# Kernel optimization log

Measured on AMD Instinct MI355X. Metric: run time of the kernel, lower is better.

Reference implementation:

```python
import jax, jax.numpy as jnp
import numpy as np

BATCH = 1024
D_MODEL = 1024
HEADS = 16
D_K = D_MODEL // HEADS  # 64


def setup_inputs() -> dict:
    key = jax.random.key(0)
    ks = jax.random.split(key, 8)
    s = 1.0 / np.sqrt(D_MODEL)
    return {
        "x": jax.random.normal(ks[0], (BATCH, D_MODEL), dtype=jnp.float32),
        "weights": jax.random.normal(ks[1], (BATCH, HEADS, D_K, D_K), dtype=jnp.float32),
        "Wq": jax.random.normal(ks[2], (D_MODEL, HEADS * D_K), dtype=jnp.float32) * s,
        "Wk": jax.random.normal(ks[3], (D_MODEL, HEADS * D_K), dtype=jnp.float32) * s,
        "Wv": jax.random.normal(ks[4], (D_MODEL, HEADS * D_K), dtype=jnp.float32) * s,
        "Wg": jax.random.normal(ks[5], (D_MODEL, HEADS), dtype=jnp.float32) * s,
        "Wo": jax.random.normal(ks[6], (D_MODEL, D_MODEL), dtype=jnp.float32) * s,
        "bo": jnp.zeros((D_MODEL,), dtype=jnp.float32),
    }


def reference(x, weights, Wq, Wk, Wv, Wg, Wo, bo):
    b = x.shape[0]
    h, dv, dk = weights.shape[1], weights.shape[2], weights.shape[3]
    # projections -> [b, h, d_k]; sigma is identity in this module
    q = (x @ Wq).reshape(b, h, dk)
    k = (x @ Wk).reshape(b, h, dk)
    v = (x @ Wv).reshape(b, h, dv)
    # gate beta: [b, h, 1]
    beta = jax.nn.sigmoid(x @ Wg)[:, :, None]
    # read existing value from fast-weight memory
    v_existing = jnp.einsum('bhvk,bhk->bhv', weights, k)
    # outer-product delta-rule write
    new_weights = weights + jnp.einsum('bhv,bhk->bhvk', beta * (v - v_existing), k)
    # read with query
    out = jnp.einsum('bhvk,bhk->bhv', new_weights, q).reshape(b, h * dv)
    out = out @ Wo + bo
    return (out, new_weights)
```

## Files before the change

### kernel.cpp

```cpp
#include <hip/hip_runtime.h>

#define BATCH 1024
#define DMODEL 1024
#define HEADS 16

typedef short bh8 __attribute__((ext_vector_type(8)));
typedef float f4 __attribute__((ext_vector_type(4)));
typedef unsigned short u16x4 __attribute__((ext_vector_type(4)));

__device__ inline unsigned short f2b(float f) {
  union { float f; unsigned int u; } x; x.f = f;
  unsigned int r = x.u + 0x7fffu + ((x.u >> 16) & 1u);
  return (unsigned short)(r >> 16);
}

__global__ __launch_bounds__(256)
void cvt_bf16_kernel(const float* __restrict__ in, unsigned short* __restrict__ out, int n4) {
  int i = blockIdx.x * 256 + threadIdx.x;
  if (i >= n4) return;
  const float4 f = ((const float4*)in)[i];
  u16x4 h = { f2b(f.x), f2b(f.y), f2b(f.z), f2b(f.w) };
  ((u16x4*)out)[i] = h;
}

__global__ __launch_bounds__(256)
void transpose_cvt_kernel(const float* __restrict__ in, unsigned short* __restrict__ out,
                          int R, int C) {
  __shared__ float t[32][33];
  int c0 = blockIdx.x * 32, r0 = blockIdx.y * 32;
  int tx = threadIdx.x, ty = threadIdx.y;
  #pragma unroll
  for (int i = ty; i < 32; i += 8)
    t[i][tx] = in[(size_t)(r0 + i) * C + c0 + tx];
  __syncthreads();
  #pragma unroll
  for (int i = ty; i < 32; i += 8)
    out[(size_t)(c0 + i) * R + r0 + tx] = f2b(t[tx][i]);
}

__global__ __launch_bounds__(256)
void beta_kernel(const float* __restrict__ x, const float* __restrict__ Wg,
                 float* __restrict__ beta) {
  __shared__ float xr[DMODEL];
  int b = blockIdx.x;
  for (int i = threadIdx.x; i < DMODEL; i += 256) xr[i] = x[(size_t)b * DMODEL + i];
  __syncthreads();
  int wid = threadIdx.x >> 6, lane = threadIdx.x & 63;
  #pragma unroll
  for (int hh = 0; hh < 4; ++hh) {
    int h = wid * 4 + hh;
    float p = 0.f;
    for (int i = lane; i < DMODEL; i += 64) p += xr[i] * Wg[(size_t)i * HEADS + h];
    #pragma unroll
    for (int off = 32; off > 0; off >>= 1) p += __shfl_down(p, off, 64);
    if (lane == 0) beta[b * HEADS + h] = 1.f / (1.f + __expf(-p));
  }
}

template<int BM, int BN>
__global__ __launch_bounds__(256)
void gemm_tn(const unsigned short* __restrict__ A, const unsigned short* __restrict__ Bt,
             float* __restrict__ C, const float* __restrict__ bias, int N, int K) {
  constexpr int BK = 32;
  constexpr int LD = BK + 8;
  constexpr int TM = BM / 32;
  constexpr int TN = BN / 32;
  __shared__ unsigned short As[BM * LD];
  __shared__ unsigned short Bs[BN * LD];
  const int tid = threadIdx.x;
  const int lane = tid & 63;
  const int wid = tid >> 6;
  const int wm = wid >> 1, wn = wid & 1;
  const int m0 = blockIdx.y * BM, n0 = blockIdx.x * BN;
  const int row16 = lane & 15;
  const int quad = lane >> 4;
  const int s_chunk = tid & 3, s_row = tid >> 2;

  f4 acc[TM][TN];
  #pragma unroll
  for (int i = 0; i < TM; ++i)
    #pragma unroll
    for (int j = 0; j < TN; ++j)
      acc[i][j] = f4{0.f, 0.f, 0.f, 0.f};

  for (int k0 = 0; k0 < K; k0 += BK) {
    #pragma unroll
    for (int p = 0; p < BM / 64; ++p) {
      int r = s_row + p * 64;
      bh8 v = *(const bh8*)(A + (size_t)(m0 + r) * K + k0 + s_chunk * 8);
      *(bh8*)(&As[r * LD + s_chunk * 8]) = v;
    }
    #pragma unroll
    for (int p = 0; p < BN / 64; ++p) {
      int r = s_row + p * 64;
      bh8 v = *(const bh8*)(Bt + (size_t)(n0 + r) * K + k0 + s_chunk * 8);
      *(bh8*)(&Bs[r * LD + s_chunk * 8]) = v;
    }
    __syncthreads();
    bh8 af[TM], bfr[TN];
    #pragma unroll
    for (int i = 0; i < TM; ++i)
      af[i] = *(const bh8*)(&As[(wm * (BM / 2) + i * 16 + row16) * LD + quad * 8]);
    #pragma unroll
    for (int j = 0; j < TN; ++j)
      bfr[j] = *(const bh8*)(&Bs[(wn * (BN / 2) + j * 16 + row16) * LD + quad * 8]);
    #pragma unroll
    for (int i = 0; i < TM; ++i)
      #pragma unroll
      for (int j = 0; j < TN; ++j)
        acc[i][j] = __builtin_amdgcn_mfma_f32_16x16x32_bf16(af[i], bfr[j], acc[i][j], 0, 0, 0);
    __syncthreads();
  }
  #pragma unroll
  for (int i = 0; i < TM; ++i) {
    #pragma unroll
    for (int j = 0; j < TN; ++j) {
      int col = n0 + wn * (BN / 2) + j * 16 + row16;
      float bv = bias ? bias[col] : 0.f;
      #pragma unroll
      for (int rg = 0; rg < 4; ++rg) {
        int row = m0 + wm * (BM / 2) + i * 16 + quad * 4 + rg;
        C[(size_t)row * N + col] = acc[i][j][rg] + bv;
      }
    }
  }
}

__global__ __launch_bounds__(256)
void fastweight_kernel(const float* __restrict__ Wf, const float* __restrict__ QKV,
                       const float* __restrict__ beta, float* __restrict__ newW,
                       unsigned short* __restrict__ hiddenh) {
  const int bh = blockIdx.x;
  const int b = bh >> 4, h = bh & 15;
  const int tid = threadIdx.x;
  const int r = tid >> 2, q4 = tid & 3;
  const float* base = QKV + (size_t)b * 3072 + h * 64;
  const float4* qp = (const float4*)base;
  const float4* kp = (const float4*)(base + 1024);
  const float* vp = base + 2048;
  const float be = beta[bh];
  const size_t woff = (size_t)bh * 4096 + (size_t)r * 64 + q4 * 16;
  const float4* wp = (const float4*)(Wf + woff);
  float4 w[4], kk[4];
  #pragma unroll
  for (int i = 0; i < 4; ++i) w[i] = wp[i];
  #pragma unroll
  for (int i = 0; i < 4; ++i) kk[i] = kp[q4 * 4 + i];
  float vex = 0.f;
  #pragma unroll
  for (int i = 0; i < 4; ++i)
    vex += w[i].x * kk[i].x + w[i].y * kk[i].y + w[i].z * kk[i].z + w[i].w * kk[i].w;
  vex += __shfl_xor(vex, 1, 64);
  vex += __shfl_xor(vex, 2, 64);
  const float dv = be * (vp[r] - vex);
  #pragma unroll
  for (int i = 0; i < 4; ++i) {
    w[i].x += dv * kk[i].x; w[i].y += dv * kk[i].y;
    w[i].z += dv * kk[i].z; w[i].w += dv * kk[i].w;
  }
  float4* op = (float4*)(newW + woff);
  #pragma unroll
  for (int i = 0; i < 4; ++i) op[i] = w[i];
  float o = 0.f;
  #pragma unroll
  for (int i = 0; i < 4; ++i) {
    float4 q = qp[q4 * 4 + i];
    o += w[i].x * q.x + w[i].y * q.y + w[i].z * q.z + w[i].w * q.w;
  }
  o += __shfl_xor(o, 1, 64);
  o += __shfl_xor(o, 2, 64);
  if (q4 == 0) hiddenh[(size_t)b * DMODEL + h * 64 + r] = f2b(o);
}

extern "C" void kernel_launch(void* const* d_in, const int* in_sizes, int n_in,
                              void* d_out, int out_size, void* d_ws, size_t ws_size,
                              hipStream_t stream) {
  const float* x  = (const float*)d_in[0];
  const float* Wf = (const float*)d_in[1];
  const float* Wq = (const float*)d_in[2];
  const float* Wk = (const float*)d_in[3];
  const float* Wv = (const float*)d_in[4];
  const float* Wg = (const float*)d_in[5];
  const float* Wo = (const float*)d_in[6];
  const float* bo = (const float*)d_in[7];
  float* out  = (float*)d_out;
  float* newW = out + (size_t)BATCH * DMODEL;

  unsigned short* xh      = (unsigned short*)d_ws;
  unsigned short* WqkvT   = xh + (size_t)1024 * 1024;
  unsigned short* WoT     = WqkvT + (size_t)3072 * 1024;
  unsigned short* hiddenh = WoT + (size_t)1024 * 1024;
  float* QKV   = (float*)(hiddenh + (size_t)1024 * 1024);
  float* betab = QKV + (size_t)1024 * 3072;

  dim3 tb(32, 8);
  cvt_bf16_kernel<<<1024, 256, 0, stream>>>(x, xh, 1024 * 1024 / 4);
  transpose_cvt_kernel<<<dim3(32, 32), tb, 0, stream>>>(Wq, WqkvT,                    1024, 1024);
  transpose_cvt_kernel<<<dim3(32, 32), tb, 0, stream>>>(Wk, WqkvT + 1024 * 1024,      1024, 1024);
  transpose_cvt_kernel<<<dim3(32, 32), tb, 0, stream>>>(Wv, WqkvT + 2 * 1024 * 1024,  1024, 1024);
  transpose_cvt_kernel<<<dim3(32, 32), tb, 0, stream>>>(Wo, WoT,                      1024, 1024);
  beta_kernel<<<BATCH, 256, 0, stream>>>(x, Wg, betab);
  gemm_tn<64, 64><<<dim3(3072 / 64, 1024 / 64), 256, 0, stream>>>(xh, WqkvT, QKV, nullptr, 3072, 1024);
  fastweight_kernel<<<BATCH * HEADS, 256, 0, stream>>>(Wf, QKV, betab, newW, hiddenh);
  gemm_tn<64, 64><<<dim3(1024 / 64, 1024 / 64), 256, 0, stream>>>(hiddenh, WoT, out, bo, 1024, 1024);
}
```

Baseline: 556.7 us.

## Merge prep kernels into one launch and coalesce fast-weight memory access

```diff
diff --git a/kernel.cpp b/kernel.cpp
--- a/kernel.cpp
+++ b/kernel.cpp
@@ -15,45 +15,47 @@
 }
 
 __global__ __launch_bounds__(256)
-void cvt_bf16_kernel(const float* __restrict__ in, unsigned short* __restrict__ out, int n4) {
-  int i = blockIdx.x * 256 + threadIdx.x;
-  if (i >= n4) return;
-  const float4 f = ((const float4*)in)[i];
-  u16x4 h = { f2b(f.x), f2b(f.y), f2b(f.z), f2b(f.w) };
-  ((u16x4*)out)[i] = h;
-}
-
-__global__ __launch_bounds__(256)
-void transpose_cvt_kernel(const float* __restrict__ in, unsigned short* __restrict__ out,
-                          int R, int C) {
-  __shared__ float t[32][33];
-  int c0 = blockIdx.x * 32, r0 = blockIdx.y * 32;
-  int tx = threadIdx.x, ty = threadIdx.y;
-  #pragma unroll
-  for (int i = ty; i < 32; i += 8)
-    t[i][tx] = in[(size_t)(r0 + i) * C + c0 + tx];
-  __syncthreads();
-  #pragma unroll
-  for (int i = ty; i < 32; i += 8)
-    out[(size_t)(c0 + i) * R + r0 + tx] = f2b(t[tx][i]);
-}
-
-__global__ __launch_bounds__(256)
-void beta_kernel(const float* __restrict__ x, const float* __restrict__ Wg,
-                 float* __restrict__ beta) {
-  __shared__ float xr[DMODEL];
-  int b = blockIdx.x;
-  for (int i = threadIdx.x; i < DMODEL; i += 256) xr[i] = x[(size_t)b * DMODEL + i];
-  __syncthreads();
-  int wid = threadIdx.x >> 6, lane = threadIdx.x & 63;
-  #pragma unroll
-  for (int hh = 0; hh < 4; ++hh) {
-    int h = wid * 4 + hh;
-    float p = 0.f;
-    for (int i = lane; i < DMODEL; i += 64) p += xr[i] * Wg[(size_t)i * HEADS + h];
-    #pragma unroll
-    for (int off = 32; off > 0; off >>= 1) p += __shfl_down(p, off, 64);
-    if (lane == 0) beta[b * HEADS + h] = 1.f / (1.f + __expf(-p));
+void prep_kernel(const float* __restrict__ x,
+                 const float* __restrict__ Wq, const float* __restrict__ Wk,
+                 const float* __restrict__ Wv, const float* __restrict__ Wo,
+                 const float* __restrict__ Wg,
+                 unsigned short* __restrict__ xh, unsigned short* __restrict__ WqkvT,
+                 unsigned short* __restrict__ WoT, float* __restrict__ betab) {
+  __shared__ float sm[32 * 33];
+  const int blk = blockIdx.x;
+  if (blk < 4096) {
+    const int mat = blk >> 10, id = blk & 1023;
+    const float* src = (mat == 0) ? Wq : (mat == 1) ? Wk : (mat == 2) ? Wv : Wo;
+    unsigned short* dst = (mat < 3) ? (WqkvT + (size_t)mat * 1024 * 1024) : WoT;
+    const int c0 = (id & 31) * 32, r0 = (id >> 5) * 32;
+    const int tx = threadIdx.x & 31, ty = threadIdx.x >> 5;
+    #pragma unroll
+    for (int i = ty; i < 32; i += 8)
+      sm[i * 33 + tx] = src[(size_t)(r0 + i) * 1024 + c0 + tx];
+    __syncthreads();
+    #pragma unroll
+    for (int i = ty; i < 32; i += 8)
+      dst[(size_t)(c0 + i) * 1024 + r0 + tx] = f2b(sm[tx * 33 + i]);
+  } else if (blk < 5120) {
+    const int i = (blk - 4096) * 256 + threadIdx.x;
+    const float4 f = ((const float4*)x)[i];
+    u16x4 hv = { f2b(f.x), f2b(f.y), f2b(f.z), f2b(f.w) };
+    ((u16x4*)xh)[i] = hv;
+  } else {
+    const int b = blk - 5120;
+    float* xr = sm;
+    for (int i = threadIdx.x; i < DMODEL; i += 256) xr[i] = x[(size_t)b * DMODEL + i];
+    __syncthreads();
+    const int wid = threadIdx.x >> 6, lane = threadIdx.x & 63;
+    #pragma unroll
+    for (int hh = 0; hh < 4; ++hh) {
+      const int h = wid * 4 + hh;
+      float p = 0.f;
+      for (int i = lane; i < DMODEL; i += 64) p += xr[i] * Wg[(size_t)i * HEADS + h];
+      #pragma unroll
+      for (int off = 32; off > 0; off >>= 1) p += __shfl_down(p, off, 64);
+      if (lane == 0) betab[b * HEADS + h] = 1.f / (1.f + __expf(-p));
+    }
   }
 }
 
@@ -132,44 +134,44 @@
                        unsigned short* __restrict__ hiddenh) {
   const int bh = blockIdx.x;
   const int b = bh >> 4, h = bh & 15;
-  const int tid = threadIdx.x;
-  const int r = tid >> 2, q4 = tid & 3;
+  const int t = threadIdx.x;
+  const int seg = t & 15;
+  const int rbase = t >> 4;
   const float* base = QKV + (size_t)b * 3072 + h * 64;
-  const float4* qp = (const float4*)base;
-  const float4* kp = (const float4*)(base + 1024);
-  const float* vp = base + 2048;
+  const float4 qq = ((const float4*)base)[seg];
+  const float4 kk = ((const float4*)(base + 1024))[seg];
   const float be = beta[bh];
-  const size_t woff = (size_t)bh * 4096 + (size_t)r * 64 + q4 * 16;
-  const float4* wp = (const float4*)(Wf + woff);
-  float4 w[4], kk[4];
-  #pragma unroll
-  for (int i = 0; i < 4; ++i) w[i] = wp[i];
-  #pragma unroll
-  for (int i = 0; i < 4; ++i) kk[i] = kp[q4 * 4 + i];
-  float vex = 0.f;
-  #pragma unroll
-  for (int i = 0; i < 4; ++i)
-    vex += w[i].x * kk[i].x + w[i].y * kk[i].y + w[i].z * kk[i].z + w[i].w * kk[i].w;
-  vex += __shfl_xor(vex, 1, 64);
-  vex += __shfl_xor(vex, 2, 64);
-  const float dv = be * (vp[r] - vex);
-  #pragma unroll
-  for (int i = 0; i < 4; ++i) {
-    w[i].x += dv * kk[i].x; w[i].y += dv * kk[i].y;
-    w[i].z += dv * kk[i].z; w[i].w += dv * kk[i].w;
-  }
-  float4* op = (float4*)(newW + woff);
-  #pragma unroll
-  for (int i = 0; i < 4; ++i) op[i] = w[i];
-  float o = 0.f;
-  #pragma unroll
-  for (int i = 0; i < 4; ++i) {
-    float4 q = qp[q4 * 4 + i];
-    o += w[i].x * q.x + w[i].y * q.y + w[i].z * q.z + w[i].w * q.w;
-  }
-  o += __shfl_xor(o, 1, 64);
-  o += __shfl_xor(o, 2, 64);
-  if (q4 == 0) hiddenh[(size_t)b * DMODEL + h * 64 + r] = f2b(o);
+  const float4* wp = (const float4*)(Wf + (size_t)bh * 4096);
+  float4* op = (float4*)(newW + (size_t)bh * 4096);
+
+  float4 w[4];
+  #pragma unroll
+  for (int j = 0; j < 4; ++j) w[j] = wp[t + 256 * j];
+
+  float vex[4];
+  #pragma unroll
+  for (int j = 0; j < 4; ++j) {
+    float p = w[j].x * kk.x + w[j].y * kk.y + w[j].z * kk.z + w[j].w * kk.w;
+    p += __shfl_xor(p, 1, 64);
+    p += __shfl_xor(p, 2, 64);
+    p += __shfl_xor(p, 4, 64);
+    p += __shfl_xor(p, 8, 64);
+    vex[j] = p;
+  }
+  #pragma unroll
+  for (int j = 0; j < 4; ++j) {
+    const int r = rbase + 16 * j;
+    const float dv = be * (base[2048 + r] - vex[j]);
+    w[j].x += dv * kk.x; w[j].y += dv * kk.y;
+    w[j].z += dv * kk.z; w[j].w += dv * kk.w;
+    op[t + 256 * j] = w[j];
+    float o = w[j].x * qq.x + w[j].y * qq.y + w[j].z * qq.z + w[j].w * qq.w;
+    o += __shfl_xor(o, 1, 64);
+    o += __shfl_xor(o, 2, 64);
+    o += __shfl_xor(o, 4, 64);
+    o += __shfl_xor(o, 8, 64);
+    if (seg == 0) hiddenh[(size_t)b * DMODEL + h * 64 + r] = f2b(o);
+  }
 }
 
 extern "C" void kernel_launch(void* const* d_in, const int* in_sizes, int n_in,
@@ -193,13 +195,7 @@
   float* QKV   = (float*)(hiddenh + (size_t)1024 * 1024);
   float* betab = QKV + (size_t)1024 * 3072;
 
-  dim3 tb(32, 8);
-  cvt_bf16_kernel<<<1024, 256, 0, stream>>>(x, xh, 1024 * 1024 / 4);
-  transpose_cvt_kernel<<<dim3(32, 32), tb, 0, stream>>>(Wq, WqkvT,                    1024, 1024);
-  transpose_cvt_kernel<<<dim3(32, 32), tb, 0, stream>>>(Wk, WqkvT + 1024 * 1024,      1024, 1024);
-  transpose_cvt_kernel<<<dim3(32, 32), tb, 0, stream>>>(Wv, WqkvT + 2 * 1024 * 1024,  1024, 1024);
-  transpose_cvt_kernel<<<dim3(32, 32), tb, 0, stream>>>(Wo, WoT,                      1024, 1024);
-  beta_kernel<<<BATCH, 256, 0, stream>>>(x, Wg, betab);
+  prep_kernel<<<6144, 256, 0, stream>>>(x, Wq, Wk, Wv, Wo, Wg, xh, WqkvT, WoT, betab);
   gemm_tn<64, 64><<<dim3(3072 / 64, 1024 / 64), 256, 0, stream>>>(xh, WqkvT, QKV, nullptr, 3072, 1024);
   fastweight_kernel<<<BATCH * HEADS, 256, 0, stream>>>(Wf, QKV, betab, newW, hiddenh);
   gemm_tn<64, 64><<<dim3(1024 / 64, 1024 / 64), 256, 0, stream>>>(hiddenh, WoT, out, bo, 1024, 1024);
```

Measured after the change: 559.9 us. About the same (+0.6%).
